# Optimization experiments

Hardware: AMD Instinct MI355X
Metric: run time of the kernel (lower is better)

Reference implementation:

```python
import jax, jax.numpy as jnp
import numpy as np

N_PED = 131072      # total pedestrians (batch)
SEG = 64            # pedestrians per segment (equal-size groups)
N_SEQ = N_PED // SEG
D_IN = 256          # enc_h_dim
D_OUT = 128         # mlp_dim


def setup_inputs() -> dict:
    key = jax.random.key(0)
    k1, k2 = jax.random.split(key, 2)
    h_states = jax.random.normal(k1, (N_PED, D_IN), dtype=jnp.float32)
    W = jax.random.normal(k2, (D_IN, D_OUT), dtype=jnp.float32) * 0.05
    b = jnp.zeros((D_OUT,), dtype=jnp.float32)
    starts = jnp.arange(N_SEQ, dtype=jnp.int64) * SEG
    seq_start_end = jnp.stack([starts, starts + SEG], axis=1)  # [N_SEQ, 2]
    return {"h_states": h_states, "W": W, "b": b, "seq_start_end": seq_start_end}


def reference(h_states, W, b, seq_start_end):
    # fc projection: (N, D_IN) -> (N, D_OUT)
    h = h_states @ W + b
    # gather each segment: equal-size groups of SEG pedestrians
    starts = seq_start_end[:, 0]                     # [G]
    idx = starts[:, None] + jnp.arange(SEG)[None, :]  # [G, S]
    seg = h[idx]                                      # [G, S, D_OUT]
    # per-segment self-attention pooling: softmax(H H^T) @ H
    scores = jnp.einsum('gsd,gtd->gst', seg, seg)     # [G, S, S]
    attn = jax.nn.softmax(scores, axis=-1)
    ctx = jnp.einsum('gst,gtd->gsd', attn, seg)       # [G, S, D_OUT]
    return ctx.reshape(-1, D_OUT)                     # [N, D_OUT]
```

## Files before the change

kernel.cpp:

```cpp
#include <hip/hip_runtime.h>
#include <stdint.h>

#define SEG 64
#define D_IN 256
#define D_OUT 128
#define NSEQ 2048

typedef __attribute__((ext_vector_type(8))) _Float16 half8;
typedef __attribute__((ext_vector_type(4))) float floatx4;

static __device__ __forceinline__ unsigned short f2h_bits(float f) {
  union { _Float16 h; unsigned short u; } v; v.h = (_Float16)f; return v.u;
}
static __device__ __forceinline__ unsigned pack2(float a, float b) {
  return (unsigned)f2h_bits(a) | ((unsigned)f2h_bits(b) << 16);
}

__global__ void prep_w_kernel(const float* __restrict__ W,
                              unsigned short* __restrict__ Wf) {
  const int idx = blockIdx.x * 256 + threadIdx.x;
  const float v = W[idx];
  const int k = idx >> 7, n = idx & 127;
  const int slot = (((n >> 4) * 8 + (k >> 5)) * 64 + ((n & 15) + 16 * ((k >> 3) & 3))) * 8 + (k & 7);
  Wf[slot] = f2h_bits(v);
}

struct SharedFrag {
  unsigned short h[4][4][64][8];
  unsigned short ht[8][2][64][8];
};

__global__ __launch_bounds__(256, 4)
void attn_fused(const float* __restrict__ hs,
                const unsigned short* __restrict__ Wf,
                const float* __restrict__ bias,
                float* __restrict__ out)
{
  __shared__ SharedFrag u;
  __shared__ unsigned short pbuf[4][2][64][8];

  const int g    = blockIdx.x;
  const int tid  = (int)threadIdx.x;
  const int w    = tid >> 6;
  const int lane = tid & 63;
  const int c    = lane & 15;
  const int q    = lane >> 4;

  floatx4 acc[8];
#pragma unroll
  for (int nt = 0; nt < 8; ++nt) {
    const float bv = bias[16 * nt + c];
    acc[nt] = (floatx4){bv, bv, bv, bv};
  }

  const float* arow = hs + ((size_t)g * SEG + 16 * w + c) * D_IN + 8 * q;
  const half8* WfV = (const half8*)Wf;
#pragma unroll
  for (int ks = 0; ks < 8; ++ks) {
    const float4 a0 = *(const float4*)(arow + 32 * ks);
    const float4 a1 = *(const float4*)(arow + 32 * ks + 4);
    union { uint4 u4; half8 h8; } cv;
    cv.u4.x = pack2(a0.x, a0.y); cv.u4.y = pack2(a0.z, a0.w);
    cv.u4.z = pack2(a1.x, a1.y); cv.u4.w = pack2(a1.z, a1.w);
    const half8 af = cv.h8;
#pragma unroll
    for (int nt = 0; nt < 8; ++nt) {
      const half8 wfv = WfV[(nt * 8 + ks) * 64 + lane];
      acc[nt] = __builtin_amdgcn_mfma_f32_16x16x32_f16(af, wfv, acc[nt], 0, 0, 0);
    }
  }

#pragma unroll
  for (int nt = 0; nt < 8; ++nt) {
    unsigned short hb[4];
#pragma unroll
    for (int i = 0; i < 4; ++i) hb[i] = f2h_bits(acc[nt][i]);
    const int lph = 16 * ((2 * nt + (c >> 3)) & 3);
#pragma unroll
    for (int i = 0; i < 4; ++i)
      u.h[w][nt >> 1][4 * q + i + lph][c & 7] = hb[i];
    const unsigned lo = (unsigned)hb[0] | ((unsigned)hb[1] << 16);
    const unsigned hi = (unsigned)hb[2] | ((unsigned)hb[3] << 16);
    *(uint2*)&u.ht[nt][w >> 1][c + 16 * ((2 * w + (q >> 1)) & 3)][4 * (q & 1)] =
        make_uint2(lo, hi);
  }

  __syncthreads();

  floatx4 sacc[4];
#pragma unroll
  for (int nt = 0; nt < 4; ++nt) sacc[nt] = (floatx4){0.f, 0.f, 0.f, 0.f};
#pragma unroll
  for (int ks = 0; ks < 4; ++ks) {
    const half8 a = *(const half8*)(&u.h[w][ks][lane][0]);
#pragma unroll
    for (int nt = 0; nt < 4; ++nt) {
      const half8 b = *(const half8*)(&u.h[nt][ks][lane][0]);
      sacc[nt] = __builtin_amdgcn_mfma_f32_16x16x32_f16(a, b, sacc[nt], 0, 0, 0);
    }
  }

  float ev[4][4];
  float inv[4];
#pragma unroll
  for (int i = 0; i < 4; ++i) {
    float m = fmaxf(fmaxf(sacc[0][i], sacc[1][i]), fmaxf(sacc[2][i], sacc[3][i]));
#pragma unroll
    for (int d = 1; d < 16; d <<= 1) m = fmaxf(m, __shfl_xor(m, d, 64));
    float ssum = 0.f;
#pragma unroll
    for (int nt = 0; nt < 4; ++nt) {
      ev[i][nt] = __expf(sacc[nt][i] - m);
      ssum += ev[i][nt];
    }
#pragma unroll
    for (int d = 1; d < 16; d <<= 1) ssum += __shfl_xor(ssum, d, 64);
    inv[i] = 1.0f / ssum;
  }

#pragma unroll
  for (int i = 0; i < 4; ++i)
#pragma unroll
    for (int nt = 0; nt < 4; ++nt)
      pbuf[w][nt >> 1][4 * q + i + 16 * ((2 * nt + (c >> 3)) & 3)][c & 7] =
          f2h_bits(ev[i][nt] * inv[i]);

  floatx4 cacc[8];
#pragma unroll
  for (int dt = 0; dt < 8; ++dt) cacc[dt] = (floatx4){0.f, 0.f, 0.f, 0.f};
#pragma unroll
  for (int kt = 0; kt < 2; ++kt) {
    const half8 pf = *(const half8*)(&pbuf[w][kt][lane][0]);
#pragma unroll
    for (int dt = 0; dt < 8; ++dt) {
      const half8 hf = *(const half8*)(&u.ht[dt][kt][lane][0]);
      cacc[dt] = __builtin_amdgcn_mfma_f32_16x16x32_f16(hf, pf, cacc[dt], 0, 0, 0);
    }
  }

  float* orow = out + ((size_t)g * SEG + 16 * w + c) * D_OUT + 4 * q;
#pragma unroll
  for (int dt = 0; dt < 8; ++dt)
    *(floatx4*)(orow + 16 * dt) = cacc[dt];
}

extern "C" void kernel_launch(void* const* d_in, const int* in_sizes, int n_in,
                              void* d_out, int out_size, void* d_ws, size_t ws_size,
                              hipStream_t stream) {
  const float* hs   = (const float*)d_in[0];
  const float* W    = (const float*)d_in[1];
  const float* bias = (const float*)d_in[2];
  float* out = (float*)d_out;
  unsigned short* Wf = (unsigned short*)d_ws;

  prep_w_kernel<<<128, 256, 0, stream>>>(W, Wf);
  attn_fused<<<NSEQ, 256, 0, stream>>>(hs, Wf, bias, out);
}
```

Baseline: 230.7 us.

## Split fused attention into projection GEMM and attention tail kernels via workspace

Splits the fused kernel into two. The first does the fc projection with register double-buffered loads of the input and weight fragments. It writes fp16 H and H-transpose fragments to workspace in MFMA-ready layout. The second kernel reads those fragments straight from global memory and does the scores, softmax and context. This is meant to cut per-block LDS use and the barrier so more blocks fit per CU, at the cost of extra global traffic (about 64 MB written and re-read) and one more launch. The old fused path is kept as a fallback when the workspace is too small.

New measurement: 249.5 us. +8.1%, slower.

```diff
diff --git a/kernel.cpp b/kernel.cpp
--- a/kernel.cpp
+++ b/kernel.cpp
@@ -23,6 +23,162 @@
   const int k = idx >> 7, n = idx & 127;
   const int slot = (((n >> 4) * 8 + (k >> 5)) * 64 + ((n & 15) + 16 * ((k >> 3) & 3))) * 8 + (k & 7);
   Wf[slot] = f2h_bits(v);
+}
+
+__global__ __launch_bounds__(256, 4)
+void gemm1_kernel(const float* __restrict__ hs,
+                  const unsigned short* __restrict__ Wf,
+                  const float* __restrict__ bias,
+                  unsigned short* __restrict__ hfrag,
+                  unsigned short* __restrict__ htfrag)
+{
+  __shared__ alignas(16) unsigned short sc[4][4096];
+  const int g    = blockIdx.x;
+  const int tid  = (int)threadIdx.x;
+  const int w    = tid >> 6;
+  const int lane = tid & 63;
+  const int c    = lane & 15;
+  const int q    = lane >> 4;
+
+  floatx4 acc[8];
+#pragma unroll
+  for (int nt = 0; nt < 8; ++nt) {
+    const float bv = bias[16 * nt + c];
+    acc[nt] = (floatx4){bv, bv, bv, bv};
+  }
+
+  const float* arow = hs + ((size_t)g * SEG + 16 * w + c) * D_IN + 8 * q;
+  const half8* WfV = (const half8*)Wf;
+
+  float4 a0[2], a1[2];
+  half8 wfb[2][8];
+  a0[0] = *(const float4*)(arow);
+  a1[0] = *(const float4*)(arow + 4);
+#pragma unroll
+  for (int nt = 0; nt < 8; ++nt) wfb[0][nt] = WfV[(nt * 8 + 0) * 64 + lane];
+
+#pragma unroll
+  for (int ks = 0; ks < 8; ++ks) {
+    const int cur = ks & 1, nx = cur ^ 1;
+    if (ks < 7) {
+      a0[nx] = *(const float4*)(arow + 32 * (ks + 1));
+      a1[nx] = *(const float4*)(arow + 32 * (ks + 1) + 4);
+#pragma unroll
+      for (int nt = 0; nt < 8; ++nt)
+        wfb[nx][nt] = WfV[(nt * 8 + ks + 1) * 64 + lane];
+    }
+    union { uint4 u4; half8 h8; } cv;
+    cv.u4.x = pack2(a0[cur].x, a0[cur].y); cv.u4.y = pack2(a0[cur].z, a0[cur].w);
+    cv.u4.z = pack2(a1[cur].x, a1[cur].y); cv.u4.w = pack2(a1[cur].z, a1[cur].w);
+    const half8 af = cv.h8;
+#pragma unroll
+    for (int nt = 0; nt < 8; ++nt)
+      acc[nt] = __builtin_amdgcn_mfma_f32_16x16x32_f16(af, wfb[cur][nt], acc[nt], 0, 0, 0);
+  }
+
+#pragma unroll
+  for (int nt = 0; nt < 8; ++nt) {
+    unsigned short hb[4];
+#pragma unroll
+    for (int i = 0; i < 4; ++i) hb[i] = f2h_bits(acc[nt][i]);
+    const int lph = 16 * ((2 * nt + (c >> 3)) & 3);
+#pragma unroll
+    for (int i = 0; i < 4; ++i)
+      sc[w][(nt >> 1) * 512 + (4 * q + i + lph) * 8 + (c & 7)] = hb[i];
+    const unsigned lo = (unsigned)hb[0] | ((unsigned)hb[1] << 16);
+    const unsigned hi = (unsigned)hb[2] | ((unsigned)hb[3] << 16);
+    *(uint2*)&sc[w][2048 + nt * 256 + (q >> 1) * 128 + c * 8 + 4 * (q & 1)] =
+        make_uint2(lo, hi);
+  }
+
+  const uint4* scv = (const uint4*)&sc[w][0];
+  uint4* gh = (uint4*)(hfrag + (size_t)(g * 4 + w) * 2048);
+#pragma unroll
+  for (int it = 0; it < 4; ++it)
+    gh[it * 64 + lane] = scv[it * 64 + lane];
+
+#pragma unroll
+  for (int it = 0; it < 4; ++it) {
+    const int dt = 2 * it + (lane >> 5);
+    const int l5 = lane & 31;
+    const size_t ghw =
+        ((size_t)((g * 8 + dt) * 2 + (w >> 1)) * 64 +
+         (lane & 15) + 16 * ((2 * w + (l5 >> 4)) & 3)) * 8;
+    *(uint4*)(htfrag + ghw) = scv[256 + dt * 32 + l5];
+  }
+}
+
+__global__ __launch_bounds__(256, 4)
+void attn_tail_kernel(const unsigned short* __restrict__ hfrag,
+                      const unsigned short* __restrict__ htfrag,
+                      float* __restrict__ out)
+{
+  __shared__ alignas(16) unsigned short pbuf[4][2][64][8];
+  const int g    = blockIdx.x;
+  const int tid  = (int)threadIdx.x;
+  const int w    = tid >> 6;
+  const int lane = tid & 63;
+  const int c    = lane & 15;
+  const int q    = lane >> 4;
+
+  const half8* hfV = (const half8*)hfrag;
+  const half8* htV = (const half8*)htfrag;
+
+  floatx4 sacc[4];
+#pragma unroll
+  for (int nt = 0; nt < 4; ++nt) sacc[nt] = (floatx4){0.f, 0.f, 0.f, 0.f};
+#pragma unroll
+  for (int ks = 0; ks < 4; ++ks) {
+    const half8 a = hfV[((size_t)(g * 4 + w) * 4 + ks) * 64 + lane];
+#pragma unroll
+    for (int nt = 0; nt < 4; ++nt) {
+      const half8 b = hfV[((size_t)(g * 4 + nt) * 4 + ks) * 64 + lane];
+      sacc[nt] = __builtin_amdgcn_mfma_f32_16x16x32_f16(a, b, sacc[nt], 0, 0, 0);
+    }
+  }
+
+  float ev[4][4];
+  float inv[4];
+#pragma unroll
+  for (int i = 0; i < 4; ++i) {
+    float m = fmaxf(fmaxf(sacc[0][i], sacc[1][i]), fmaxf(sacc[2][i], sacc[3][i]));
+#pragma unroll
+    for (int d = 1; d < 16; d <<= 1) m = fmaxf(m, __shfl_xor(m, d, 64));
+    float ssum = 0.f;
+#pragma unroll
+    for (int nt = 0; nt < 4; ++nt) {
+      ev[i][nt] = __expf(sacc[nt][i] - m);
+      ssum += ev[i][nt];
+    }
+#pragma unroll
+    for (int d = 1; d < 16; d <<= 1) ssum += __shfl_xor(ssum, d, 64);
+    inv[i] = 1.0f / ssum;
+  }
+
+#pragma unroll
+  for (int i = 0; i < 4; ++i)
+#pragma unroll
+    for (int nt = 0; nt < 4; ++nt)
+      pbuf[w][nt >> 1][4 * q + i + 16 * ((2 * nt + (c >> 3)) & 3)][c & 7] =
+          f2h_bits(ev[i][nt] * inv[i]);
+
+  floatx4 cacc[8];
+#pragma unroll
+  for (int dt = 0; dt < 8; ++dt) cacc[dt] = (floatx4){0.f, 0.f, 0.f, 0.f};
+#pragma unroll
+  for (int kt = 0; kt < 2; ++kt) {
+    const half8 pf = *(const half8*)(&pbuf[w][kt][lane][0]);
+#pragma unroll
+    for (int dt = 0; dt < 8; ++dt) {
+      const half8 hf = htV[((size_t)(g * 8 + dt) * 2 + kt) * 64 + lane];
+      cacc[dt] = __builtin_amdgcn_mfma_f32_16x16x32_f16(hf, pf, cacc[dt], 0, 0, 0);
+    }
+  }
+
+  float* orow = out + ((size_t)g * SEG + 16 * w + c) * D_OUT + 4 * q;
+#pragma unroll
+  for (int dt = 0; dt < 8; ++dt)
+    *(floatx4*)(orow + 16 * dt) = cacc[dt];
 }
 
 struct SharedFrag {
@@ -151,8 +307,17 @@
   const float* W    = (const float*)d_in[1];
   const float* bias = (const float*)d_in[2];
   float* out = (float*)d_out;
+
   unsigned short* Wf = (unsigned short*)d_ws;
-
   prep_w_kernel<<<128, 256, 0, stream>>>(W, Wf);
-  attn_fused<<<NSEQ, 256, 0, stream>>>(hs, Wf, bias, out);
-}
+
+  const size_t need = (size_t)(1 + 32 + 32) << 20;
+  if (ws_size >= need + (1 << 20)) {
+    unsigned short* hfrag  = (unsigned short*)((char*)d_ws + ((size_t)1 << 20));
+    unsigned short* htfrag = (unsigned short*)((char*)d_ws + ((size_t)33 << 20));
+    gemm1_kernel<<<NSEQ, 256, 0, stream>>>(hs, Wf, bias, hfrag, htfrag);
+    attn_tail_kernel<<<NSEQ, 256, 0, stream>>>(hfrag, htfrag, out);
+  } else {
+    attn_fused<<<NSEQ, 256, 0, stream>>>(hs, Wf, bias, out);
+  }
+}
```
